# Kernel tuning notes

Measured on AMD Instinct MI355X. Metric: run time of the kernel, lower is better.

Reference implementation:

```python
import jax, jax.numpy as jnp
import numpy as np

N = 100000   # nodes
E = 1600000  # edges
DIN, DH, DOUT = 64, 128, 128


def setup_inputs() -> dict:
    key = jax.random.key(0)
    ks = jax.random.split(key, 12)
    x = jax.random.normal(ks[0], (N, DIN), dtype=jnp.float32)
    edge_index = jax.random.randint(ks[1], (2, E), 0, N, dtype=jnp.int32)
    s = 1.0 / np.sqrt(DIN)
    W1 = jax.random.uniform(ks[2], (DIN, DH), jnp.float32, -s, s)
    b1 = jnp.zeros((DH,), jnp.float32)
    g1 = jnp.ones((DH,), jnp.float32)
    bt1 = jnp.zeros((DH,), jnp.float32)
    s2 = 1.0 / np.sqrt(DH)
    W2 = jax.random.uniform(ks[3], (DH, DOUT), jnp.float32, -s2, s2)
    b2 = jnp.zeros((DOUT,), jnp.float32)
    g2 = jnp.ones((DOUT,), jnp.float32)
    bt2 = jnp.zeros((DOUT,), jnp.float32)
    return {"x": x, "edge_index": edge_index, "W1": W1, "b1": b1, "g1": g1,
            "bt1": bt1, "W2": W2, "b2": b2, "g2": g2, "bt2": bt2}


def _layer_norm(h, g, b, eps=1e-5):
    mu = h.mean(-1, keepdims=True)
    var = h.var(-1, keepdims=True)
    return (h - mu) * jax.lax.rsqrt(var + eps) * g + b


def reference(x, edge_index, W1, b1, g1, bt1, W2, b2, g2, bt2):
    # GCN normalization with self-loops (shared graph structure for both layers)
    src, dst = edge_index[0], edge_index[1]
    loops = jnp.arange(N, dtype=src.dtype)
    src = jnp.concatenate([src, loops])
    dst = jnp.concatenate([dst, loops])
    deg = jax.ops.segment_sum(jnp.ones_like(src, jnp.float32), dst, num_segments=N)
    dinv = jnp.where(deg > 0, jax.lax.rsqrt(deg), 0.0)
    norm = dinv[src] * dinv[dst]  # [E+N]

    def gcn(h, W, b):
        hw = h @ W                         # linear first (PyG GCNConv)
        msg = hw[src] * norm[:, None]      # gather + edge scale
        return jax.ops.segment_sum(msg, dst, num_segments=N) + b

    h = jax.nn.relu(_layer_norm(gcn(x, W1, b1), g1, bt1))
    # dropout is identity at inference
    h = jax.nn.relu(_layer_norm(gcn(h, W2, b2), g2, bt2))
    return h
```

## Files before the change

kernel.cpp:

```cpp
#include <hip/hip_runtime.h>

#define NN 100000
#define NE 1600000
#define NBKT 196
#define CAP 12288
#define EPB 2048
#define ABLK ((NE + EPB - 1) / EPB)
typedef unsigned short u16;
typedef unsigned int u32;

typedef __attribute__((ext_vector_type(8))) short short8v;
typedef __attribute__((ext_vector_type(4))) float f32x4;

__device__ __forceinline__ u32 f2bf(float f) {
    u32 u = __float_as_uint(f);
    return (u + 0x7fffu + ((u >> 16) & 1u)) >> 16;
}
__device__ __forceinline__ u32 pack2(float a, float b) {
    return f2bf(a) | (f2bf(b) << 16);
}
__device__ __forceinline__ void accum8(float* a, uint4 u, float w) {
    a[0] += __uint_as_float(u.x << 16) * w;
    a[1] += __uint_as_float(u.x & 0xffff0000u) * w;
    a[2] += __uint_as_float(u.y << 16) * w;
    a[3] += __uint_as_float(u.y & 0xffff0000u) * w;
    a[4] += __uint_as_float(u.z << 16) * w;
    a[5] += __uint_as_float(u.z & 0xffff0000u) * w;
    a[6] += __uint_as_float(u.w << 16) * w;
    a[7] += __uint_as_float(u.w & 0xffff0000u) * w;
}

__global__ __launch_bounds__(256) void kA_bin(const int* __restrict__ src,
                                              const int* __restrict__ dst,
                                              int* __restrict__ gcnt,
                                              u32* __restrict__ binned) {
    __shared__ int bc[NBKT];
    __shared__ int cbase[NBKT];
    const int tid = threadIdx.x;
    for (int i = tid; i < NBKT; i += 256) bc[i] = 0;
    __syncthreads();
    const int e0 = blockIdx.x * EPB;
#pragma unroll
    for (int i = 0; i < EPB / 256; ++i) {
        const int e = e0 + i * 256 + tid;
        if (e < NE) atomicAdd(&bc[dst[e] >> 9], 1);
    }
    __syncthreads();
    for (int i = tid; i < NBKT; i += 256)
        cbase[i] = bc[i] ? atomicAdd(&gcnt[i], bc[i]) : 0;
    __syncthreads();
    for (int i = tid; i < NBKT; i += 256) bc[i] = 0;
    __syncthreads();
#pragma unroll
    for (int i = 0; i < EPB / 256; ++i) {
        const int e = e0 + i * 256 + tid;
        if (e < NE) {
            const int d = dst[e];
            const int bkt = d >> 9;
            const int p = atomicAdd(&bc[bkt], 1);
            binned[bkt * CAP + cbase[bkt] + p] = ((u32)src[e] << 9) | (u32)(d & 511);
        }
    }
}

__global__ __launch_bounds__(256) void kB_fill(const u32* __restrict__ binned,
                                               const int* __restrict__ gcnt,
                                               int2* __restrict__ off2,
                                               float* __restrict__ dinv,
                                               int* __restrict__ csr,
                                               const float* __restrict__ x,
                                               u16* __restrict__ xb) {
    __shared__ int lcnt[512];
    __shared__ int lpos[512];
    __shared__ float sdinv[512];
    __shared__ int ws[4];
    const int b = blockIdx.x;
    const int tid = threadIdx.x;
    const int cnt = gcnt[b];
    const int base0 = b * CAP;
    const int node0 = b << 9;
    lcnt[tid] = 0;
    lcnt[tid + 256] = 0;
    __syncthreads();
    for (int e = tid; e < cnt; e += 256)
        atomicAdd(&lcnt[binned[base0 + e] & 511], 1);
    __syncthreads();
    const int c0 = lcnt[tid * 2], c1 = lcnt[tid * 2 + 1];
    const int s = c0 + c1;
    const int lane = tid & 63, w = tid >> 6;
    int incl = s;
#pragma unroll
    for (int o = 1; o < 64; o <<= 1) {
        const int u = __shfl_up(incl, o);
        if (lane >= o) incl += u;
    }
    if (lane == 63) ws[w] = incl;
    __syncthreads();
    int base = incl - s;
    for (int i = 0; i < w; ++i) base += ws[i];
    lpos[tid * 2] = base;
    lpos[tid * 2 + 1] = base + c0;
    const float d0 = rsqrtf(1.0f + (float)c0);
    const float d1 = rsqrtf(1.0f + (float)c1);
    sdinv[tid * 2] = d0;
    sdinv[tid * 2 + 1] = d1;
    const int n0 = node0 + tid * 2;
    if (n0 < NN) {
        off2[n0] = make_int2(base0 + base, base0 + base + c0);
        dinv[n0] = d0;
    }
    if (n0 + 1 < NN) {
        off2[n0 + 1] = make_int2(base0 + base + c0, base0 + base + c0 + c1);
        dinv[n0 + 1] = d1;
    }
    __syncthreads();
    for (int e = tid; e < cnt; e += 256) {
        const u32 u = binned[base0 + e];
        const int p = atomicAdd(&lpos[u & 511], 1);
        csr[base0 + p] = (int)(u >> 9);
    }
    const int nmax = min(512, NN - node0);
    for (int gi = tid; gi < nmax * 8; gi += 256) {
        const int nl = gi >> 3, ch = gi & 7;
        const float dr = sdinv[nl];
        const size_t xo = (size_t)(node0 + nl) * 64 + ch * 8;
        const float4 v0 = *(const float4*)&x[xo];
        const float4 v1 = *(const float4*)&x[xo + 4];
        uint4 o;
        o.x = pack2(v0.x * dr, v0.y * dr); o.y = pack2(v0.z * dr, v0.w * dr);
        o.z = pack2(v1.x * dr, v1.y * dr); o.w = pack2(v1.z * dr, v1.w * dr);
        *(uint4*)&xb[xo] = o;
    }
}

__global__ __launch_bounds__(256) void k_prep(const float* __restrict__ W1,
                                              const float* __restrict__ W2,
                                              u16* __restrict__ WT1,
                                              u16* __restrict__ WT2,
                                              int* __restrict__ gcnt) {
    const int i = blockIdx.x * 256 + threadIdx.x;
    if (i < 8192) {
        const int k = i >> 7, c = i & 127;
        WT1[c * 64 + k] = (u16)f2bf(W1[i]);
    } else if (i < 24576) {
        const int i2 = i - 8192;
        const int k = i2 >> 7, c = i2 & 127;
        WT2[c * 128 + k] = (u16)f2bf(W2[i2]);
    } else if (i < 24576 + NBKT) {
        gcnt[i - 24576] = 0;
    }
}

template<int K, bool FP32OUT, bool PRESCALE>
__global__ __launch_bounds__(256) void k_fused(const u16* __restrict__ A,
                                               const int2* __restrict__ off2,
                                               const int* __restrict__ csr,
                                               const float* __restrict__ dinv,
                                               const u16* __restrict__ WT,
                                               const float* __restrict__ bias,
                                               const float* __restrict__ g,
                                               const float* __restrict__ bt,
                                               void* __restrict__ outp) {
    constexpr int RB = K * 2;
    constexpr int SUBS = 512 / K;
    constexpr int LSH = (K == 64) ? 7 : 8;
    __shared__ u16 As[32 * K];
    __shared__ float s1s[4][32];
    __shared__ float s2s[4][32];
    __shared__ int claim;
    const int tid = threadIdx.x;
    const int wv = tid >> 6, lane = tid & 63;
    const int sub = lane / (64 / SUBS);
    const int l = lane & (64 / SUBS - 1);
    const char* Ab = (const char*)A + ((u32)l << 4);
    const int nodeBase = blockIdx.x * 32;

    if (tid == 0) claim = 0;
    __syncthreads();

    int i;
    if (lane == 0) i = atomicAdd(&claim, 1);
    i = __builtin_amdgcn_readfirstlane(i);
    while (i < 32) {
        const int node = nodeBase + i;
        const float di = dinv[node];
        float a[8] = {};
        {
            const uint4 u = *(const uint4*)(Ab + ((u32)node << LSH));
            accum8(a, u, (sub == 0) ? 1.0f : 0.0f);
        }
        const int2 oe = off2[node];
        int base = oe.x;
        const int e1 = oe.y;
        u32 iA = 0, iB = 0, iC = 0;
        float vA = 0.f, vB = 0.f, vC = 0.f;
        if (base < e1) {
            const int eA = base + sub, eB = eA + SUBS, eC = eA + 2 * SUBS;
            iA = (u32)csr[min(eA, e1 - 1)];
            iB = (u32)csr[min(eB, e1 - 1)];
            iC = (u32)csr[min(eC, e1 - 1)];
            vA = (eA < e1) ? 1.f : 0.f;
            vB = (eB < e1) ? 1.f : 0.f;
            vC = (eC < e1) ? 1.f : 0.f;
        }
        while (base < e1) {
            const uint4 uA = *(const uint4*)(Ab + (iA << LSH));
            const uint4 uB = *(const uint4*)(Ab + (iB << LSH));
            const uint4 uC = *(const uint4*)(Ab + (iC << LSH));
            const float wA = vA, wB = vB, wC = vC;
            base += 3 * SUBS;
            if (base < e1) {
                const int eA = base + sub, eB = eA + SUBS, eC = eA + 2 * SUBS;
                iA = (u32)csr[min(eA, e1 - 1)];
                iB = (u32)csr[min(eB, e1 - 1)];
                iC = (u32)csr[min(eC, e1 - 1)];
                vA = (eA < e1) ? 1.f : 0.f;
                vB = (eB < e1) ? 1.f : 0.f;
                vC = (eC < e1) ? 1.f : 0.f;
            }
            accum8(a, uA, wA);
            accum8(a, uB, wB);
            accum8(a, uC, wC);
        }
#pragma unroll
        for (int t = 0; t < 8; ++t)
#pragma unroll
            for (int o = 64 / SUBS; o < 64; o <<= 1)
                a[t] += __shfl_xor(a[t], o);
        if (sub == 0) {
            uint4 o;
            o.x = pack2(a[0] * di, a[1] * di); o.y = pack2(a[2] * di, a[3] * di);
            o.z = pack2(a[4] * di, a[5] * di); o.w = pack2(a[6] * di, a[7] * di);
            *(uint4*)((char*)As + i * RB + (((u32)l << 4) ^ ((u32)(i & 7) << 4))) = o;
        }
        if (lane == 0) i = atomicAdd(&claim, 1);
        i = __builtin_amdgcn_readfirstlane(i);
    }
    __syncthreads();

    const int lr = lane & 15, kg = lane >> 4;
    short8v af[2][K / 32];
#pragma unroll
    for (int rt = 0; rt < 2; ++rt)
#pragma unroll
        for (int kk = 0; kk < K / 32; ++kk)
            af[rt][kk] = *(const short8v*)((const char*)As + (rt * 16 + lr) * RB +
                                           ((u32)(kk * 64 + kg * 16) ^ ((u32)(lr & 7) << 4)));
    f32x4 acc[2][2];
    float bv[2], gv[2], tv[2];
#pragma unroll
    for (int nt = 0; nt < 2; ++nt) {
        acc[0][nt] = (f32x4){0.f, 0.f, 0.f, 0.f};
        acc[1][nt] = (f32x4){0.f, 0.f, 0.f, 0.f};
        const int col = wv * 32 + nt * 16 + lr;
        short8v bf[K / 32];
#pragma unroll
        for (int kk = 0; kk < K / 32; ++kk)
            bf[kk] = *(const short8v*)&WT[col * K + kk * 32 + kg * 8];
#pragma unroll
        for (int rt = 0; rt < 2; ++rt)
#pragma unroll
            for (int kk = 0; kk < K / 32; ++kk)
                acc[rt][nt] = __builtin_amdgcn_mfma_f32_16x16x32_bf16(
                    af[rt][kk], bf[kk], acc[rt][nt], 0, 0, 0);
        bv[nt] = bias[col]; gv[nt] = g[col]; tv[nt] = bt[col];
    }

    float s1[2][4] = {};
    float s2[2][4] = {};
#pragma unroll
    for (int rt = 0; rt < 2; ++rt)
#pragma unroll
        for (int nt = 0; nt < 2; ++nt)
#pragma unroll
            for (int j = 0; j < 4; ++j) {
                const float v = acc[rt][nt][j] + bv[nt];
                acc[rt][nt][j] = v;
                s1[rt][j] += v;
                s2[rt][j] += v * v;
            }
#pragma unroll
    for (int rt = 0; rt < 2; ++rt)
#pragma unroll
        for (int j = 0; j < 4; ++j)
#pragma unroll
            for (int o = 1; o < 16; o <<= 1) {
                s1[rt][j] += __shfl_xor(s1[rt][j], o);
                s2[rt][j] += __shfl_xor(s2[rt][j], o);
            }
    if (lr == 0) {
#pragma unroll
        for (int rt = 0; rt < 2; ++rt)
#pragma unroll
            for (int j = 0; j < 4; ++j) {
                s1s[wv][rt * 16 + kg * 4 + j] = s1[rt][j];
                s2s[wv][rt * 16 + kg * 4 + j] = s2[rt][j];
            }
    }
    __syncthreads();

#pragma unroll
    for (int rt = 0; rt < 2; ++rt)
#pragma unroll
        for (int j = 0; j < 4; ++j) {
            const int row = rt * 16 + kg * 4 + j;
            const float t1 = s1s[0][row] + s1s[1][row] + s1s[2][row] + s1s[3][row];
            const float t2 = s2s[0][row] + s2s[1][row] + s2s[2][row] + s2s[3][row];
            const float mu = t1 * (1.0f / 128.0f);
            const float var = t2 * (1.0f / 128.0f) - mu * mu;
            const float rs = rsqrtf(var + 1e-5f);
            const int node = nodeBase + row;
            const float dr = PRESCALE ? dinv[node] : 1.0f;
#pragma unroll
            for (int nt = 0; nt < 2; ++nt) {
                const float y = fmaxf((acc[rt][nt][j] - mu) * rs * gv[nt] + tv[nt], 0.f) * dr;
                const int col = wv * 32 + nt * 16 + lr;
                if constexpr (FP32OUT)
                    ((float*)outp)[(size_t)node * 128 + col] = y;
                else
                    ((u16*)outp)[(size_t)node * 128 + col] = (u16)f2bf(y);
            }
        }
}

extern "C" void kernel_launch(void* const* d_in, const int* in_sizes, int n_in,
                              void* d_out, int out_size, void* d_ws, size_t ws_size,
                              hipStream_t stream) {
    const float* x   = (const float*)d_in[0];
    const int*   ei  = (const int*)d_in[1];
    const float* W1  = (const float*)d_in[2];
    const float* b1  = (const float*)d_in[3];
    const float* g1  = (const float*)d_in[4];
    const float* bt1 = (const float*)d_in[5];
    const float* W2  = (const float*)d_in[6];
    const float* b2  = (const float*)d_in[7];
    const float* g2  = (const float*)d_in[8];
    const float* bt2 = (const float*)d_in[9];

    const int* src = ei;
    const int* dst = ei + NE;

    const int NP = (NN + 255) & ~255;
    int*   gcnt   = (int*)d_ws;
    int2*  off2   = (int2*)(gcnt + 256);
    float* dinv   = (float*)(off2 + NP);
    int*   csr    = (int*)(dinv + NP);
    u32*   binned = (u32*)(csr + NBKT * CAP);
    u16*   xb     = (u16*)(binned + NBKT * CAP);
    u16*   h1     = xb + (size_t)NN * 64;
    u16*   WT1    = h1 + (size_t)NN * 128;
    u16*   WT2    = WT1 + 128 * 64;

    k_prep<<<(24576 + NBKT + 255) / 256, 256, 0, stream>>>(W1, W2, WT1, WT2, gcnt);
    kA_bin<<<ABLK, 256, 0, stream>>>(src, dst, gcnt, binned);
    kB_fill<<<NBKT, 256, 0, stream>>>(binned, gcnt, off2, dinv, csr, x, xb);

    k_fused<64, false, true><<<NN / 32, 256, 0, stream>>>(
        xb, off2, csr, dinv, WT1, b1, g1, bt1, h1);

    k_fused<128, true, false><<<NN / 32, 256, 0, stream>>>(
        h1, off2, csr, dinv, WT2, b2, g2, bt2, d_out);
}
```

Measured before the change: 201.2 us.

## Split layer-2 fused kernel into separate aggregation and GEMM+LayerNorm kernels

```diff
diff --git a/kernel.cpp b/kernel.cpp
--- a/kernel.cpp
+++ b/kernel.cpp
@@ -4,7 +4,7 @@
 #define NE 1600000
 #define NBKT 196
 #define CAP 12288
-#define EPB 2048
+#define EPB 8192
 #define ABLK ((NE + EPB - 1) / EPB)
 typedef unsigned short u16;
 typedef unsigned int u32;
@@ -323,6 +323,159 @@
         }
 }
 
+__global__ __launch_bounds__(256) void k_agg128(const u16* __restrict__ A,
+                                                const int2* __restrict__ off2,
+                                                const int* __restrict__ csr,
+                                                const float* __restrict__ dinv,
+                                                u16* __restrict__ out) {
+    const int node = blockIdx.x * 4 + (threadIdx.x >> 6);
+    const int lane = threadIdx.x & 63;
+    const int sub = lane >> 4, l = lane & 15;
+    const char* Ab = (const char*)A + ((u32)l << 4);
+    const float di = dinv[node];
+    float a[8] = {};
+    {
+        const uint4 u = *(const uint4*)(Ab + ((u32)node << 8));
+        accum8(a, u, (sub == 0) ? 1.0f : 0.0f);
+    }
+    const int2 oe = off2[node];
+    int base = oe.x;
+    const int e1 = oe.y;
+    u32 iA = 0, iB = 0, iC = 0;
+    float vA = 0.f, vB = 0.f, vC = 0.f;
+    if (base < e1) {
+        const int eA = base + sub, eB = eA + 4, eC = eA + 8;
+        iA = (u32)csr[min(eA, e1 - 1)];
+        iB = (u32)csr[min(eB, e1 - 1)];
+        iC = (u32)csr[min(eC, e1 - 1)];
+        vA = (eA < e1) ? 1.f : 0.f;
+        vB = (eB < e1) ? 1.f : 0.f;
+        vC = (eC < e1) ? 1.f : 0.f;
+    }
+    while (base < e1) {
+        const uint4 uA = *(const uint4*)(Ab + (iA << 8));
+        const uint4 uB = *(const uint4*)(Ab + (iB << 8));
+        const uint4 uC = *(const uint4*)(Ab + (iC << 8));
+        const float wA = vA, wB = vB, wC = vC;
+        base += 12;
+        if (base < e1) {
+            const int eA = base + sub, eB = eA + 4, eC = eA + 8;
+            iA = (u32)csr[min(eA, e1 - 1)];
+            iB = (u32)csr[min(eB, e1 - 1)];
+            iC = (u32)csr[min(eC, e1 - 1)];
+            vA = (eA < e1) ? 1.f : 0.f;
+            vB = (eB < e1) ? 1.f : 0.f;
+            vC = (eC < e1) ? 1.f : 0.f;
+        }
+        accum8(a, uA, wA);
+        accum8(a, uB, wB);
+        accum8(a, uC, wC);
+    }
+#pragma unroll
+    for (int i = 0; i < 8; ++i) {
+        a[i] += __shfl_xor(a[i], 16);
+        a[i] += __shfl_xor(a[i], 32);
+    }
+    if (sub == 0) {
+        uint4 o;
+        o.x = pack2(a[0] * di, a[1] * di); o.y = pack2(a[2] * di, a[3] * di);
+        o.z = pack2(a[4] * di, a[5] * di); o.w = pack2(a[6] * di, a[7] * di);
+        *(uint4*)((char*)out + ((u32)node << 8) + ((u32)l << 4)) = o;
+    }
+}
+
+template<int K, bool FP32OUT, bool PRESCALE>
+__global__ __launch_bounds__(256) void k_gemm_ln(const u16* __restrict__ Ain,
+                                                 const u16* __restrict__ WT,
+                                                 const float* __restrict__ bias,
+                                                 const float* __restrict__ g,
+                                                 const float* __restrict__ bt,
+                                                 const float* __restrict__ dinv,
+                                                 void* __restrict__ outp) {
+    const int tid = threadIdx.x;
+    const int wv = tid >> 6, lane = tid & 63;
+    const int lr = lane & 15, kg = lane >> 4;
+    const int row0 = blockIdx.x * 128 + wv * 32;
+
+    short8v af[2][K / 32];
+#pragma unroll
+    for (int rt = 0; rt < 2; ++rt) {
+        const int r = min(row0 + rt * 16 + lr, NN - 1);
+#pragma unroll
+        for (int kk = 0; kk < K / 32; ++kk)
+            af[rt][kk] = *(const short8v*)&Ain[(size_t)r * K + kk * 32 + kg * 8];
+    }
+    f32x4 acc[2][8];
+#pragma unroll
+    for (int rt = 0; rt < 2; ++rt)
+#pragma unroll
+        for (int nt = 0; nt < 8; ++nt)
+            acc[rt][nt] = (f32x4){0.f, 0.f, 0.f, 0.f};
+
+#pragma unroll
+    for (int nt = 0; nt < 8; ++nt) {
+        const int col = nt * 16 + lr;
+        short8v bf[K / 32];
+#pragma unroll
+        for (int kk = 0; kk < K / 32; ++kk)
+            bf[kk] = *(const short8v*)&WT[col * K + kk * 32 + kg * 8];
+#pragma unroll
+        for (int rt = 0; rt < 2; ++rt)
+#pragma unroll
+            for (int kk = 0; kk < K / 32; ++kk)
+                acc[rt][nt] = __builtin_amdgcn_mfma_f32_16x16x32_bf16(
+                    af[rt][kk], bf[kk], acc[rt][nt], 0, 0, 0);
+    }
+
+    float bv[8], gv[8], tv[8];
+#pragma unroll
+    for (int nt = 0; nt < 8; ++nt) {
+        const int col = nt * 16 + lr;
+        bv[nt] = bias[col]; gv[nt] = g[col]; tv[nt] = bt[col];
+    }
+
+#pragma unroll
+    for (int rt = 0; rt < 2; ++rt) {
+        float s1[4] = {0.f, 0.f, 0.f, 0.f};
+        float s2[4] = {0.f, 0.f, 0.f, 0.f};
+#pragma unroll
+        for (int nt = 0; nt < 8; ++nt)
+#pragma unroll
+            for (int j = 0; j < 4; ++j) {
+                const float v = acc[rt][nt][j] + bv[nt];
+                acc[rt][nt][j] = v;
+                s1[j] += v;
+                s2[j] += v * v;
+            }
+#pragma unroll
+        for (int j = 0; j < 4; ++j)
+#pragma unroll
+            for (int o = 1; o < 16; o <<= 1) {
+                s1[j] += __shfl_xor(s1[j], o);
+                s2[j] += __shfl_xor(s2[j], o);
+            }
+#pragma unroll
+        for (int j = 0; j < 4; ++j) {
+            const int r = row0 + rt * 16 + kg * 4 + j;
+            const float mu = s1[j] * (1.0f / 128.0f);
+            const float var = s2[j] * (1.0f / 128.0f) - mu * mu;
+            const float rs = rsqrtf(var + 1e-5f);
+            if (r < NN) {
+                const float dr = PRESCALE ? dinv[r] : 1.0f;
+#pragma unroll
+                for (int nt = 0; nt < 8; ++nt) {
+                    const float y = fmaxf((acc[rt][nt][j] - mu) * rs * gv[nt] + tv[nt], 0.f) * dr;
+                    const int col = nt * 16 + lr;
+                    if constexpr (FP32OUT)
+                        ((float*)outp)[(size_t)r * 128 + col] = y;
+                    else
+                        ((u16*)outp)[(size_t)r * 128 + col] = (u16)f2bf(y);
+                }
+            }
+        }
+    }
+}
+
 extern "C" void kernel_launch(void* const* d_in, const int* in_sizes, int n_in,
                               void* d_out, int out_size, void* d_ws, size_t ws_size,
                               hipStream_t stream) {
@@ -347,9 +500,10 @@
     int*   csr    = (int*)(dinv + NP);
     u32*   binned = (u32*)(csr + NBKT * CAP);
     u16*   xb     = (u16*)(binned + NBKT * CAP);
-    u16*   h1     = xb + (size_t)NN * 64;
-    u16*   WT1    = h1 + (size_t)NN * 128;
+    u16*   aggh   = xb + (size_t)NN * 64;
+    u16*   WT1    = aggh + (size_t)NN * 128;
     u16*   WT2    = WT1 + 128 * 64;
+    u16*   h1     = (u16*)d_out;
 
     k_prep<<<(24576 + NBKT + 255) / 256, 256, 0, stream>>>(W1, W2, WT1, WT2, gcnt);
     kA_bin<<<ABLK, 256, 0, stream>>>(src, dst, gcnt, binned);
@@ -358,6 +512,7 @@
     k_fused<64, false, true><<<NN / 32, 256, 0, stream>>>(
         xb, off2, csr, dinv, WT1, b1, g1, bt1, h1);
 
-    k_fused<128, true, false><<<NN / 32, 256, 0, stream>>>(
-        h1, off2, csr, dinv, WT2, b2, g2, bt2, d_out);
-}
+    k_agg128<<<NN / 4, 256, 0, stream>>>(h1, off2, csr, dinv, aggh);
+    k_gemm_ln<128, true, false><<<(NN + 127) / 128, 256, 0, stream>>>(
+        aggh, WT2, b2, g2, bt2, dinv, d_out);
+}
```

Result: slower. 209.7 us (+4.2%).
